# Kernel tuning notes

Hardware: AMD Instinct MI355X
Metric: run time of the kernel (lower is better)

The kernel has to match this reference:

```python
import jax, jax.numpy as jnp
import numpy as np

NBLOCK = 2000
DIM = 2048
B, T = 32, 1024
EPS = 1e-12  # F.normalize eps


def _l2norm(v, axis):
    n = jnp.sqrt(jnp.sum(v * v, axis=axis, keepdims=True))
    return v / jnp.maximum(n, EPS)


def setup_inputs() -> dict:
    key = jax.random.key(0)
    kx, km, kw = jax.random.split(key, 3)
    x = jax.random.normal(kx, (B, T, DIM), dtype=jnp.float32)
    mask = jax.random.randint(km, (B, T), 0, 2).astype(jnp.int32)
    stdv = 1.0 / np.sqrt(DIM)
    weight = jax.random.uniform(kw, (NBLOCK, DIM), dtype=jnp.float32,
                                minval=-stdv, maxval=stdv)
    return {"x": x, "mask": mask, "weight": weight}


def reference(x, mask, weight):
    half = x.shape[0] // 2
    nblock = weight.shape[0]
    m = mask.astype(x.dtype)  # [B, T]

    # diversity: || W W^T - I ||_F
    gram = weight @ weight.T  # [N, N]
    diversity_loss = jnp.linalg.norm(gram - jnp.eye(nblock, dtype=weight.dtype))

    # cosine-similarity attention: [B, T, N]
    att = jnp.einsum('btd,nd->btn', _l2norm(x, axis=2), _l2norm(weight, axis=1))

    # uniformity loss: masked sum over T, softmax over blocks, mean over half-batch
    s = jnp.einsum('btn,bt->nb', att[:half], m[:half])  # [N, half]
    tmp = jnp.mean(jax.nn.softmax(s, axis=0), axis=1)   # [N]
    u_loss = jnp.linalg.norm(tmp)

    # per-row min over masked positions of the top-1 similarity
    top1 = jnp.max(att, axis=2)  # [B, T] (only topk[...,0] is used)
    inf = jnp.asarray(jnp.inf, dtype=x.dtype)
    masked_top1 = jnp.where(m > 0, top1, inf)
    min_sim = jnp.min(masked_top1[:half], axis=1)   # [half]
    ab_min = jnp.min(masked_top1[half:], axis=1)    # [half]

    return (0.2 * diversity_loss,
            2.0 - jnp.mean(min_sim) + jnp.mean(ab_min),
            0.5 * u_loss)
```

## Files before the change

kernel.cpp:

```cpp
#include <hip/hip_runtime.h>

typedef unsigned short u16;
typedef unsigned int u32;
typedef __attribute__((ext_vector_type(8))) short short8;
typedef __attribute__((ext_vector_type(8))) u16 ushort8;
typedef __attribute__((ext_vector_type(4))) u16 ushort4_t;
typedef __attribute__((ext_vector_type(4))) float fx4;

#define DIMK 2048
#define NBLK 2000

typedef const __attribute__((address_space(1))) void* gp_t;
typedef __attribute__((address_space(3))) void* lp_t;

__device__ __forceinline__ u16 f2bf(float f) {
  u32 u = __float_as_uint(f);
  u32 r = (u + 0x7fffu + ((u >> 16) & 1u)) >> 16;
  return (u16)r;
}

__device__ __forceinline__ u32 fkey(float f) {
  u32 u = __float_as_uint(f);
  return (u & 0x80000000u) ? ~u : (u | 0x80000000u);
}
__device__ __forceinline__ float dekey(u32 k) {
  u32 u = (k & 0x80000000u) ? (k ^ 0x80000000u) : ~k;
  return __uint_as_float(u);
}

__device__ __forceinline__ void ring_gemm128(const u16* gA0, const u16* gA1,
                                             const u16* gB0, const u16* gB1,
                                             u16 (*ring)[2][4096],
                                             int wv, int wr, int wc, int fIntra,
                                             fx4 acc[4][4])
{
#pragma unroll
  for (int mi = 0; mi < 4; mi++)
#pragma unroll
    for (int ni = 0; ni < 4; ni++)
      acc[mi][ni] = fx4{0.f, 0.f, 0.f, 0.f};

#define STG(kt)                                                                  \
  do {                                                                           \
    const int ko_ = (kt) << 5;                                                   \
    u16* lA_ = &ring[(kt) % 3][0][wv << 10];                                     \
    u16* lB_ = &ring[(kt) % 3][1][wv << 10];                                     \
    __builtin_amdgcn_global_load_lds((gp_t)(gA0 + ko_), (lp_t)lA_,         16, 0, 0); \
    __builtin_amdgcn_global_load_lds((gp_t)(gA1 + ko_), (lp_t)(lA_ + 512), 16, 0, 0); \
    __builtin_amdgcn_global_load_lds((gp_t)(gB0 + ko_), (lp_t)lB_,         16, 0, 0); \
    __builtin_amdgcn_global_load_lds((gp_t)(gB1 + ko_), (lp_t)(lB_ + 512), 16, 0, 0); \
  } while (0)

  STG(0);
  STG(1);

  const int NT = DIMK / 32;
#pragma unroll 1
  for (int t = 0; t < NT; ++t) {
    if (t + 2 < NT) {
      STG(t + 2);
      asm volatile("s_waitcnt vmcnt(8)" ::: "memory");
    } else if (t + 1 < NT) {
      asm volatile("s_waitcnt vmcnt(4)" ::: "memory");
    } else {
      asm volatile("s_waitcnt vmcnt(0)" ::: "memory");
    }
    __builtin_amdgcn_s_barrier();

    const u16* lAt = &ring[t % 3][0][0];
    const u16* lBt = &ring[t % 3][1][0];
    short8 af[4], bfr[4];
#pragma unroll
    for (int ni = 0; ni < 4; ni++)
      bfr[ni] = *(const short8*)(lBt + (wc * 4 + ni) * 512 + fIntra);
#pragma unroll
    for (int mi = 0; mi < 4; mi++)
      af[mi] = *(const short8*)(lAt + (wr * 4 + mi) * 512 + fIntra);

    __builtin_amdgcn_s_setprio(1);
#pragma unroll
    for (int mi = 0; mi < 4; mi++)
#pragma unroll
      for (int ni = 0; ni < 4; ni++)
        acc[mi][ni] = __builtin_amdgcn_mfma_f32_16x16x32_bf16(af[mi], bfr[ni], acc[mi][ni], 0, 0, 0);
    __builtin_amdgcn_s_setprio(0);
    __builtin_amdgcn_s_barrier();
  }
#undef STG
}

__global__ __launch_bounds__(256) void norm_rows_x(const float* __restrict__ x,
                                                   u16* __restrict__ Xn)
{
  const int wv = threadIdx.x >> 6, lane = threadIdx.x & 63;
  const int row = blockIdx.x * 4 + wv;
  const float4* xr = (const float4*)(x + (size_t)row * DIMK);
  float4 v[8];
  float ss = 0.f;
#pragma unroll
  for (int j = 0; j < 8; j++) {
    v[j] = xr[j * 64 + lane];
    ss += v[j].x*v[j].x + v[j].y*v[j].y + v[j].z*v[j].z + v[j].w*v[j].w;
  }
#pragma unroll
  for (int off = 1; off < 64; off <<= 1) ss += __shfl_xor(ss, off);
  float inv = 1.0f / fmaxf(sqrtf(ss), 1e-12f);
  ushort4_t* o = (ushort4_t*)(Xn + (size_t)row * DIMK);
#pragma unroll
  for (int j = 0; j < 8; j++) {
    ushort4_t t;
    t[0] = f2bf(v[j].x * inv); t[1] = f2bf(v[j].y * inv);
    t[2] = f2bf(v[j].z * inv); t[3] = f2bf(v[j].w * inv);
    o[j * 64 + lane] = t;
  }
}

__global__ __launch_bounds__(256) void norm_rows_w(const float* __restrict__ w,
                                                   u16* __restrict__ Wn,
                                                   u16* __restrict__ Wb)
{
  const int wv = threadIdx.x >> 6, lane = threadIdx.x & 63;
  const int row = blockIdx.x * 4 + wv;
  ushort4_t* on_ = (ushort4_t*)(Wn + (size_t)row * DIMK);
  ushort4_t* ob_ = (ushort4_t*)(Wb + (size_t)row * DIMK);
  if (row < NBLK) {
    const float4* wr_ = (const float4*)(w + (size_t)row * DIMK);
    float4 v[8];
    float ss = 0.f;
#pragma unroll
    for (int j = 0; j < 8; j++) {
      v[j] = wr_[j * 64 + lane];
      ss += v[j].x*v[j].x + v[j].y*v[j].y + v[j].z*v[j].z + v[j].w*v[j].w;
    }
#pragma unroll
    for (int off = 1; off < 64; off <<= 1) ss += __shfl_xor(ss, off);
    float inv = 1.0f / fmaxf(sqrtf(ss), 1e-12f);
#pragma unroll
    for (int j = 0; j < 8; j++) {
      ushort4_t tn, tb;
      tn[0] = f2bf(v[j].x * inv); tn[1] = f2bf(v[j].y * inv);
      tn[2] = f2bf(v[j].z * inv); tn[3] = f2bf(v[j].w * inv);
      tb[0] = f2bf(v[j].x); tb[1] = f2bf(v[j].y);
      tb[2] = f2bf(v[j].z); tb[3] = f2bf(v[j].w);
      on_[j * 64 + lane] = tn;
      ob_[j * 64 + lane] = tb;
    }
  } else {
    ushort4_t z = ushort4_t{0, 0, 0, 0};
#pragma unroll
    for (int j = 0; j < 8; j++) { on_[j * 64 + lane] = z; ob_[j * 64 + lane] = z; }
  }
}

__global__ __launch_bounds__(256) void gram_kernel(const u16* __restrict__ Wb,
                                                   float* __restrict__ divsum)
{
  const int bx = blockIdx.x, by = blockIdx.y;
  if (by > bx) return;
  __shared__ __align__(16) u16 ring[3][2][4096];
  const int tid = threadIdx.x, wv = tid >> 6, lane = tid & 63;
  const int wr = wv & 1, wc = wv >> 1, quad = lane >> 4, lc = lane & 15;
  const int i0 = by * 128, j0 = bx * 128;

  const int srow = wv * 32 + (lane >> 2);
  const int skel = (((lane & 3) ^ ((lane >> 3) & 3)) << 3);
  const u16* gA0 = Wb + (size_t)(i0 + srow) * DIMK + skel;
  const u16* gA1 = gA0 + (size_t)16 * DIMK;
  const u16* gB0 = Wb + (size_t)(j0 + srow) * DIMK + skel;
  const u16* gB1 = gB0 + (size_t)16 * DIMK;
  const int fIntra = lc * 32 + ((quad ^ ((lc >> 1) & 3)) << 3);

  fx4 acc[4][4];
  ring_gemm128(gA0, gA1, gB0, gB1, ring, wv, wr, wc, fIntra, acc);

  const float mult = (bx == by) ? 1.0f : 2.0f;
  float local = 0.f;
#pragma unroll
  for (int mi = 0; mi < 4; mi++) {
#pragma unroll
    for (int ni = 0; ni < 4; ni++) {
#pragma unroll
      for (int r = 0; r < 4; r++) {
        int i = i0 + wr * 64 + mi * 16 + quad * 4 + r;
        int j = j0 + wc * 64 + ni * 16 + lc;
        float g = acc[mi][ni][r];
        float d = (i == j && i < NBLK) ? 1.0f : 0.0f;
        float e = g - d;
        local += e * e;
      }
    }
  }
  local *= mult;
#pragma unroll
  for (int off = 1; off < 64; off <<= 1) local += __shfl_xor(local, off);
  if (lane == 0) atomicAdd(divsum, local);
}

__global__ __launch_bounds__(256) void att_kernel(const u16* __restrict__ Xn,
                                                  const u16* __restrict__ Wn,
                                                  const int* __restrict__ mask,
                                                  u32* __restrict__ top1k,
                                                  float* __restrict__ s)
{
  __shared__ __align__(16) u16 ring[3][2][4096];
  const int orig = blockIdx.x;
  const int wg   = ((orig & 7) << 9) | (orig >> 3);
  const int xb   = wg & 15;
  const int yb   = wg >> 4;
  const int row0 = yb << 7, col0 = xb << 7;

  const int tid = threadIdx.x, wv = tid >> 6, lane = tid & 63;
  const int wr = wv & 1, wc = wv >> 1, quad = lane >> 4, lc = lane & 15;

  const int srow = wv * 32 + (lane >> 2);
  const int skel = (((lane & 3) ^ ((lane >> 3) & 3)) << 3);
  const u16* gA0 = Xn + (size_t)(row0 + srow) * DIMK + skel;
  const u16* gA1 = gA0 + (size_t)16 * DIMK;
  const u16* gB0 = Wn + (size_t)(col0 + srow) * DIMK + skel;
  const u16* gB1 = gB0 + (size_t)16 * DIMK;
  const int fIntra = lc * 32 + ((quad ^ ((lc >> 1) & 3)) << 3);

  fx4 acc[4][4];
  ring_gemm128(gA0, gA1, gB0, gB1, ring, wv, wr, wc, fIntra, acc);

#pragma unroll
  for (int mi = 0; mi < 4; mi++) {
#pragma unroll
    for (int r = 0; r < 4; r++) {
      float v = -3.0e38f;
#pragma unroll
      for (int ni = 0; ni < 4; ni++) {
        int col = col0 + wc * 64 + ni * 16 + lc;
        float av = acc[mi][ni][r];
        v = (col < NBLK && av > v) ? av : v;
      }
      v = fmaxf(v, __shfl_xor(v, 1));
      v = fmaxf(v, __shfl_xor(v, 2));
      v = fmaxf(v, __shfl_xor(v, 4));
      v = fmaxf(v, __shfl_xor(v, 8));
      if (lc == 0) {
        int row = row0 + wr * 64 + mi * 16 + quad * 4 + r;
        atomicMax(&top1k[row], fkey(v));
      }
    }
  }

  if (yb < 128) {
    const int b = yb >> 3;
    float sv[4] = {0.f, 0.f, 0.f, 0.f};
#pragma unroll
    for (int mi = 0; mi < 4; mi++) {
#pragma unroll
      for (int r = 0; r < 4; r++) {
        float mval = (float)mask[row0 + wr * 64 + mi * 16 + quad * 4 + r];
#pragma unroll
        for (int ni = 0; ni < 4; ni++)
          sv[ni] += mval * acc[mi][ni][r];
      }
    }
#pragma unroll
    for (int ni = 0; ni < 4; ni++) {
      float v = sv[ni];
      v += __shfl_xor(v, 16);
      v += __shfl_xor(v, 32);
      int col = col0 + wc * 64 + ni * 16 + lc;
      if (quad == 0 && col < NBLK)
        atomicAdd(&s[b * 2048 + col], v);
    }
  }
}

__global__ __launch_bounds__(256) void softmax_kernel(const float* __restrict__ s,
                                                      float* __restrict__ tmp)
{
  const int b = blockIdx.x, tid = threadIdx.x;
  const float* sb = s + b * 2048;
  __shared__ float red[4];
  float mx = -3.0e38f;
  for (int n = tid; n < NBLK; n += 256) mx = fmaxf(mx, sb[n]);
#pragma unroll
  for (int off = 1; off < 64; off <<= 1) mx = fmaxf(mx, __shfl_xor(mx, off));
  if ((tid & 63) == 0) red[tid >> 6] = mx;
  __syncthreads();
  mx = fmaxf(fmaxf(red[0], red[1]), fmaxf(red[2], red[3]));
  __syncthreads();
  float se = 0.f;
  for (int n = tid; n < NBLK; n += 256) se += expf(sb[n] - mx);
#pragma unroll
  for (int off = 1; off < 64; off <<= 1) se += __shfl_xor(se, off);
  if ((tid & 63) == 0) red[tid >> 6] = se;
  __syncthreads();
  se = red[0] + red[1] + red[2] + red[3];
  float scale = 1.0f / (se * 16.0f);
  for (int n = tid; n < NBLK; n += 256) atomicAdd(&tmp[n], expf(sb[n] - mx) * scale);
}

__global__ __launch_bounds__(1024) void finalize_kernel(const u32* __restrict__ top1k,
                                                        const int* __restrict__ mask,
                                                        const float* __restrict__ tmp,
                                                        const float* __restrict__ divsum,
                                                        float* __restrict__ out)
{
  const int tid = threadIdx.x;
  __shared__ float sMin[32];
  __shared__ float sSq[16];
  const int b = tid >> 5, li = tid & 31;
  float mn = 3.0e38f;
  for (int t = li; t < 1024; t += 32) {
    int idx = b * 1024 + t;
    if (mask[idx] > 0) mn = fminf(mn, dekey(top1k[idx]));
  }
#pragma unroll
  for (int off = 1; off < 32; off <<= 1) mn = fminf(mn, __shfl_xor(mn, off));
  if (li == 0) sMin[b] = mn;
  float ssq = 0.f;
  for (int n = tid; n < NBLK; n += 1024) { float v = tmp[n]; ssq += v * v; }
#pragma unroll
  for (int off = 1; off < 64; off <<= 1) ssq += __shfl_xor(ssq, off);
  if ((tid & 63) == 0) sSq[tid >> 6] = ssq;
  __syncthreads();
  if (tid == 0) {
    float m0 = 0.f, m1 = 0.f;
    for (int i = 0; i < 16; i++) { m0 += sMin[i]; m1 += sMin[16 + i]; }
    m0 *= (1.0f / 16.0f); m1 *= (1.0f / 16.0f);
    float sq = 0.f;
    for (int i = 0; i < 16; i++) sq += sSq[i];
    out[0] = 0.2f * sqrtf(divsum[0]);
    out[1] = 2.0f - m0 + m1;
    out[2] = 0.5f * sqrtf(sq);
  }
}

extern "C" void kernel_launch(void* const* d_in, const int* in_sizes, int n_in,
                              void* d_out, int out_size, void* d_ws, size_t ws_size,
                              hipStream_t stream) {
  const float* x    = (const float*)d_in[0];
  const int*   mask = (const int*)d_in[1];
  const float* w    = (const float*)d_in[2];
  float* out = (float*)d_out;

  char* ws = (char*)d_ws;
  u32*   top1k  = (u32*)(ws);
  float* s      = (float*)(ws + 131072);
  float* tmp    = (float*)(ws + 262144);
  float* divsum = (float*)(ws + 270336);
  u16*   Xn     = (u16*)(ws + 270592);
  u16*   Wn     = (u16*)(ws + 270592 + 134217728ull);
  u16*   Wb     = (u16*)(ws + 270592 + 134217728ull + 8388608ull);

  hipMemsetAsync(ws, 0, 270592, stream);

  norm_rows_w<<<dim3(512), dim3(256), 0, stream>>>(w, Wn, Wb);
  norm_rows_x<<<dim3(8192), dim3(256), 0, stream>>>(x, Xn);
  gram_kernel<<<dim3(16, 16), dim3(256), 0, stream>>>(Wb, divsum);
  att_kernel<<<dim3(4096), dim3(256), 0, stream>>>(Xn, Wn, mask, top1k, s);
  softmax_kernel<<<dim3(16), dim3(256), 0, stream>>>(s, tmp);
  finalize_kernel<<<dim3(1), dim3(1024), 0, stream>>>(top1k, mask, tmp, divsum, out);
}
```

Baseline: 773.7 us.

## Widen attention GEMM tile to 128x256 and fuse softmax into finalize kernel

The attention GEMM now gives each workgroup a 128x256 output tile instead of 128x128, using its own inline triple-buffered global-to-LDS pipeline with 8 B-fragments per wave. The block-to-tile mapping is reworked for XCD locality. This halves the number of workgroups and the re-reads of the X operand, but raises accumulator register pressure (128 floats per thread) and LDS use. The softmax and finalize kernels are merged into one single-block tail kernel, which drops a launch and the tmp atomics.

```diff
diff --git a/kernel.cpp b/kernel.cpp
--- a/kernel.cpp
+++ b/kernel.cpp
@@ -196,32 +196,90 @@
   if (lane == 0) atomicAdd(divsum, local);
 }
 
-__global__ __launch_bounds__(256) void att_kernel(const u16* __restrict__ Xn,
-                                                  const u16* __restrict__ Wn,
-                                                  const int* __restrict__ mask,
-                                                  u32* __restrict__ top1k,
-                                                  float* __restrict__ s)
-{
-  __shared__ __align__(16) u16 ring[3][2][4096];
-  const int orig = blockIdx.x;
-  const int wg   = ((orig & 7) << 9) | (orig >> 3);
-  const int xb   = wg & 15;
-  const int yb   = wg >> 4;
-  const int row0 = yb << 7, col0 = xb << 7;
+__global__ __launch_bounds__(256, 2) void att_kernel(const u16* __restrict__ Xn,
+                                                     const u16* __restrict__ Wn,
+                                                     const int* __restrict__ mask,
+                                                     u32* __restrict__ top1k,
+                                                     float* __restrict__ s)
+{
+  __shared__ __align__(16) u16 ring[3][12288];
+
+  const int orig  = blockIdx.x;
+  const int xcd   = orig & 7;
+  const int local = orig >> 3;
+  const int yb    = xcd * 32 + ((local >> 5) << 2) + (local & 3);
+  const int xb    = (local >> 2) & 7;
+  const int row0 = yb << 7, col0 = xb << 8;
 
   const int tid = threadIdx.x, wv = tid >> 6, lane = tid & 63;
-  const int wr = wv & 1, wc = wv >> 1, quad = lane >> 4, lc = lane & 15;
-
-  const int srow = wv * 32 + (lane >> 2);
+  const int wr = wv >> 1, wc = wv & 1, quad = lane >> 4, lc = lane & 15;
+
+  const int srow = lane >> 2;
   const int skel = (((lane & 3) ^ ((lane >> 3) & 3)) << 3);
-  const u16* gA0 = Xn + (size_t)(row0 + srow) * DIMK + skel;
+  const u16* gA0 = Xn + (size_t)(row0 + wv * 32 + srow) * DIMK + skel;
   const u16* gA1 = gA0 + (size_t)16 * DIMK;
-  const u16* gB0 = Wn + (size_t)(col0 + srow) * DIMK + skel;
+  const u16* gB0 = Wn + (size_t)(col0 + wv * 64 + srow) * DIMK + skel;
   const u16* gB1 = gB0 + (size_t)16 * DIMK;
+  const u16* gB2 = gB0 + (size_t)32 * DIMK;
+  const u16* gB3 = gB0 + (size_t)48 * DIMK;
   const int fIntra = lc * 32 + ((quad ^ ((lc >> 1) & 3)) << 3);
 
-  fx4 acc[4][4];
-  ring_gemm128(gA0, gA1, gB0, gB1, ring, wv, wr, wc, fIntra, acc);
+  fx4 acc[4][8];
+#pragma unroll
+  for (int mi = 0; mi < 4; mi++)
+#pragma unroll
+    for (int ni = 0; ni < 8; ni++)
+      acc[mi][ni] = fx4{0.f, 0.f, 0.f, 0.f};
+
+#define STG6(kt)                                                                 \
+  do {                                                                           \
+    const int ko_ = (kt) << 5;                                                   \
+    u16* lA_ = &ring[(kt) % 3][wv << 10];                                        \
+    u16* lB_ = &ring[(kt) % 3][4096 + (wv << 11)];                               \
+    __builtin_amdgcn_global_load_lds((gp_t)(gA0 + ko_), (lp_t)lA_,          16, 0, 0); \
+    __builtin_amdgcn_global_load_lds((gp_t)(gA1 + ko_), (lp_t)(lA_ + 512),  16, 0, 0); \
+    __builtin_amdgcn_global_load_lds((gp_t)(gB0 + ko_), (lp_t)lB_,          16, 0, 0); \
+    __builtin_amdgcn_global_load_lds((gp_t)(gB1 + ko_), (lp_t)(lB_ + 512),  16, 0, 0); \
+    __builtin_amdgcn_global_load_lds((gp_t)(gB2 + ko_), (lp_t)(lB_ + 1024), 16, 0, 0); \
+    __builtin_amdgcn_global_load_lds((gp_t)(gB3 + ko_), (lp_t)(lB_ + 1536), 16, 0, 0); \
+  } while (0)
+
+  STG6(0);
+  STG6(1);
+
+  const int NT = DIMK / 32;
+#pragma unroll 1
+  for (int t = 0; t < NT; ++t) {
+    if (t + 2 < NT) {
+      STG6(t + 2);
+      asm volatile("s_waitcnt vmcnt(12)" ::: "memory");
+    } else if (t + 1 < NT) {
+      asm volatile("s_waitcnt vmcnt(6)" ::: "memory");
+    } else {
+      asm volatile("s_waitcnt vmcnt(0)" ::: "memory");
+    }
+    __builtin_amdgcn_s_barrier();
+
+    const u16* lAt = &ring[t % 3][0];
+    const u16* lBt = &ring[t % 3][0] + 4096;
+    short8 af[4], bfr[8];
+#pragma unroll
+    for (int ni = 0; ni < 8; ni++)
+      bfr[ni] = *(const short8*)(lBt + (wc * 8 + ni) * 512 + fIntra);
+#pragma unroll
+    for (int mi = 0; mi < 4; mi++)
+      af[mi] = *(const short8*)(lAt + (wr * 4 + mi) * 512 + fIntra);
+
+    __builtin_amdgcn_s_setprio(1);
+#pragma unroll
+    for (int mi = 0; mi < 4; mi++)
+#pragma unroll
+      for (int ni = 0; ni < 8; ni++)
+        acc[mi][ni] = __builtin_amdgcn_mfma_f32_16x16x32_bf16(af[mi], bfr[ni], acc[mi][ni], 0, 0, 0);
+    __builtin_amdgcn_s_setprio(0);
+    __builtin_amdgcn_s_barrier();
+  }
+#undef STG6
 
 #pragma unroll
   for (int mi = 0; mi < 4; mi++) {
@@ -229,8 +287,8 @@
     for (int r = 0; r < 4; r++) {
       float v = -3.0e38f;
 #pragma unroll
-      for (int ni = 0; ni < 4; ni++) {
-        int col = col0 + wc * 64 + ni * 16 + lc;
+      for (int ni = 0; ni < 8; ni++) {
+        int col = col0 + wc * 128 + ni * 16 + lc;
         float av = acc[mi][ni][r];
         v = (col < NBLK && av > v) ? av : v;
       }
@@ -247,63 +305,65 @@
 
   if (yb < 128) {
     const int b = yb >> 3;
-    float sv[4] = {0.f, 0.f, 0.f, 0.f};
+    float sv[8] = {0.f, 0.f, 0.f, 0.f, 0.f, 0.f, 0.f, 0.f};
 #pragma unroll
     for (int mi = 0; mi < 4; mi++) {
 #pragma unroll
       for (int r = 0; r < 4; r++) {
         float mval = (float)mask[row0 + wr * 64 + mi * 16 + quad * 4 + r];
 #pragma unroll
-        for (int ni = 0; ni < 4; ni++)
+        for (int ni = 0; ni < 8; ni++)
           sv[ni] += mval * acc[mi][ni][r];
       }
     }
 #pragma unroll
-    for (int ni = 0; ni < 4; ni++) {
+    for (int ni = 0; ni < 8; ni++) {
       float v = sv[ni];
       v += __shfl_xor(v, 16);
       v += __shfl_xor(v, 32);
-      int col = col0 + wc * 64 + ni * 16 + lc;
+      int col = col0 + wc * 128 + ni * 16 + lc;
       if (quad == 0 && col < NBLK)
         atomicAdd(&s[b * 2048 + col], v);
     }
   }
 }
 
-__global__ __launch_bounds__(256) void softmax_kernel(const float* __restrict__ s,
-                                                      float* __restrict__ tmp)
-{
-  const int b = blockIdx.x, tid = threadIdx.x;
-  const float* sb = s + b * 2048;
-  __shared__ float red[4];
+__global__ __launch_bounds__(1024) void tail_kernel(const float* __restrict__ s,
+                                                    const u32* __restrict__ top1k,
+                                                    const int* __restrict__ mask,
+                                                    const float* __restrict__ divsum,
+                                                    float* __restrict__ out)
+{
+  const int tid = threadIdx.x;
+  const int w = tid >> 6, lane = tid & 63;
+  __shared__ float mx_s[16], ise_s[16];
+  __shared__ float red[16];
+  __shared__ float sMin[32];
+
+  const float* sb = s + w * 2048;
   float mx = -3.0e38f;
-  for (int n = tid; n < NBLK; n += 256) mx = fmaxf(mx, sb[n]);
+  for (int n = lane; n < NBLK; n += 64) mx = fmaxf(mx, sb[n]);
 #pragma unroll
   for (int off = 1; off < 64; off <<= 1) mx = fmaxf(mx, __shfl_xor(mx, off));
-  if ((tid & 63) == 0) red[tid >> 6] = mx;
+  float se = 0.f;
+  for (int n = lane; n < NBLK; n += 64) se += expf(sb[n] - mx);
+#pragma unroll
+  for (int off = 1; off < 64; off <<= 1) se += __shfl_xor(se, off);
+  if (lane == 0) { mx_s[w] = mx; ise_s[w] = 1.0f / (se * 16.0f); }
   __syncthreads();
-  mx = fmaxf(fmaxf(red[0], red[1]), fmaxf(red[2], red[3]));
-  __syncthreads();
-  float se = 0.f;
-  for (int n = tid; n < NBLK; n += 256) se += expf(sb[n] - mx);
-#pragma unroll
-  for (int off = 1; off < 64; off <<= 1) se += __shfl_xor(se, off);
-  if ((tid & 63) == 0) red[tid >> 6] = se;
-  __syncthreads();
-  se = red[0] + red[1] + red[2] + red[3];
-  float scale = 1.0f / (se * 16.0f);
-  for (int n = tid; n < NBLK; n += 256) atomicAdd(&tmp[n], expf(sb[n] - mx) * scale);
-}
-
-__global__ __launch_bounds__(1024) void finalize_kernel(const u32* __restrict__ top1k,
-                                                        const int* __restrict__ mask,
-                                                        const float* __restrict__ tmp,
-                                                        const float* __restrict__ divsum,
-                                                        float* __restrict__ out)
-{
-  const int tid = threadIdx.x;
-  __shared__ float sMin[32];
-  __shared__ float sSq[16];
+
+  float ssq = 0.f;
+  for (int n = tid; n < NBLK; n += 1024) {
+    float v = 0.f;
+#pragma unroll
+    for (int b = 0; b < 16; b++)
+      v += expf(s[b * 2048 + n] - mx_s[b]) * ise_s[b];
+    ssq += v * v;
+  }
+#pragma unroll
+  for (int off = 1; off < 64; off <<= 1) ssq += __shfl_xor(ssq, off);
+  if (lane == 0) red[w] = ssq;
+
   const int b = tid >> 5, li = tid & 31;
   float mn = 3.0e38f;
   for (int t = li; t < 1024; t += 32) {
@@ -313,18 +373,14 @@
 #pragma unroll
   for (int off = 1; off < 32; off <<= 1) mn = fminf(mn, __shfl_xor(mn, off));
   if (li == 0) sMin[b] = mn;
-  float ssq = 0.f;
-  for (int n = tid; n < NBLK; n += 1024) { float v = tmp[n]; ssq += v * v; }
-#pragma unroll
-  for (int off = 1; off < 64; off <<= 1) ssq += __shfl_xor(ssq, off);
-  if ((tid & 63) == 0) sSq[tid >> 6] = ssq;
   __syncthreads();
+
   if (tid == 0) {
     float m0 = 0.f, m1 = 0.f;
     for (int i = 0; i < 16; i++) { m0 += sMin[i]; m1 += sMin[16 + i]; }
     m0 *= (1.0f / 16.0f); m1 *= (1.0f / 16.0f);
     float sq = 0.f;
-    for (int i = 0; i < 16; i++) sq += sSq[i];
+    for (int i = 0; i < 16; i++) sq += red[i];
     out[0] = 0.2f * sqrtf(divsum[0]);
     out[1] = 2.0f - m0 + m1;
     out[2] = 0.5f * sqrtf(sq);
@@ -342,7 +398,6 @@
   char* ws = (char*)d_ws;
   u32*   top1k  = (u32*)(ws);
   float* s      = (float*)(ws + 131072);
-  float* tmp    = (float*)(ws + 262144);
   float* divsum = (float*)(ws + 270336);
   u16*   Xn     = (u16*)(ws + 270592);
   u16*   Wn     = (u16*)(ws + 270592 + 134217728ull);
@@ -353,7 +408,6 @@
   norm_rows_w<<<dim3(512), dim3(256), 0, stream>>>(w, Wn, Wb);
   norm_rows_x<<<dim3(8192), dim3(256), 0, stream>>>(x, Xn);
   gram_kernel<<<dim3(16, 16), dim3(256), 0, stream>>>(Wb, divsum);
-  att_kernel<<<dim3(4096), dim3(256), 0, stream>>>(Xn, Wn, mask, top1k, s);
-  softmax_kernel<<<dim3(16), dim3(256), 0, stream>>>(s, tmp);
-  finalize_kernel<<<dim3(1), dim3(1024), 0, stream>>>(top1k, mask, tmp, divsum, out);
-}
+  att_kernel<<<dim3(2048), dim3(256), 0, stream>>>(Xn, Wn, mask, top1k, s);
+  tail_kernel<<<dim3(1), dim3(1024), 0, stream>>>(s, top1k, mask, divsum, out);
+}
```

Result: faster. 724.7 us (-6.3%).
